# Kernel optimization log

Measured on AMD Instinct MI355X. Metric: run time of the kernel, lower is better.

Reference implementation:

```python
import jax, jax.numpy as jnp
import numpy as np

H = 64  # GRU hidden size


def _gru_scan(x_proj, m, U, b_rec):
    # x_proj: [S,B,3H] precomputed input projections (time-major); m: [S,B] bool mask
    B = x_proj.shape[1]
    h0 = jnp.zeros((B, H), x_proj.dtype)

    def step(h, inp):
        xp, mt = inp
        rec = h @ U + b_rec                       # [B,3H] (Keras reset_after=True)
        xz, xr, xh = jnp.split(xp, 3, axis=-1)
        rz, rr, rh = jnp.split(rec, 3, axis=-1)
        z = jax.nn.sigmoid(xz + rz)
        r = jax.nn.sigmoid(xr + rr)
        hh = jnp.tanh(xh + r * rh)
        hn = z * h + (1.0 - z) * hh
        hn = jnp.where(mt[:, None], hn, h)        # masked steps carry state through
        return hn, hn

    hT, hs = jax.lax.scan(step, h0, (x_proj, m))
    return hs, hT  # hs: [S,B,H], hT: [B,H]


def setup_inputs() -> dict:
    key = jax.random.key(0)
    ks = jax.random.split(key, 16)
    V, E = 50000, 25
    B, S, T = 512, 200, 10
    s = 0.05
    f32 = jnp.float32
    inp = {
        "input_batch": jax.random.randint(ks[0], (B, S, T), 0, V),
        "emb_table": jax.random.normal(ks[1], (V, E), f32) * s,
        "W_f": jax.random.normal(ks[2], (E, 3 * H), f32) * s,
        "U_f": jax.random.normal(ks[3], (H, 3 * H), f32) * s,
        "b_f": jnp.zeros((2, 3 * H), f32),
        "W_b": jax.random.normal(ks[4], (E, 3 * H), f32) * s,
        "U_b": jax.random.normal(ks[5], (H, 3 * H), f32) * s,
        "b_b": jnp.zeros((2, 3 * H), f32),
        "W_k": jax.random.normal(ks[6], (2 * H, H), f32) * s,
        "b_k": jnp.zeros((H,), f32),
        "W_q": jax.random.normal(ks[7], (H, H), f32) * s,
        "b_q": jnp.zeros((H,), f32),
        "W_e": jax.random.normal(ks[8], (H, 1), f32) * s,
        "b_e": jnp.zeros((1,), f32),
    }
    return inp


def reference(input_batch, emb_table, W_f, U_f, b_f, W_b, U_b, b_b, W_k, b_k, W_q, b_q, W_e, b_e):
    mask = input_batch != 0                                  # [B,S,T]
    emb = emb_table[input_batch]                             # [B,S,T,E]
    nm = mask.astype(emb.dtype)
    denom = nm.sum(axis=2)                                   # [B,S]
    denom = jnp.where(denom == 0, jnp.ones_like(denom), denom)
    x = (emb * nm[..., None]).sum(axis=2) / denom[..., None] # [B,S,E] masked mean over tags
    step_mask = mask[:, :, 0]                                # [B,S] GRU step mask

    xT = jnp.swapaxes(x, 0, 1)                               # [S,B,E]
    mT = jnp.swapaxes(step_mask, 0, 1)                       # [S,B]

    # forward GRU
    hs_f, hT_f = _gru_scan(xT @ W_f + b_f[0], mT, U_f, b_f[1])
    # backward GRU: reverse time, scan, reverse back
    hs_b, _ = _gru_scan((xT @ W_b + b_b[0])[::-1], mT[::-1], U_b, b_b[1])
    hs_b = hs_b[::-1]

    out = jnp.swapaxes(jnp.concatenate([hs_f, hs_b], axis=-1), 0, 1)  # [B,S,2H]

    # Bahdanau attention; query = forward final state
    keys = out @ W_k + b_k                                   # [B,S,H]
    queries = hT_f @ W_q + b_q                               # [B,H]
    e = jnp.tanh(keys + queries[:, None, :]) @ W_e + b_e     # [B,S,1]
    e = e + (1.0 - step_mask.astype(e.dtype))[..., None] * -1e9
    w = jax.nn.softmax(e, axis=1)                            # [B,S,1]
    context = (w * out).sum(axis=1)                          # [B,2H]
    return context
```

## Files before the change

### kernel.cpp

```cpp
#include <hip/hip_runtime.h>
#include <math.h>

#define BATCH 512
#define SEQ   200
#define TOK   10
#define EMB   25
#define XPAD  28
#define HID   64
#define G3    192

__device__ __forceinline__ float fast_sigmoid(float t) {
    float e = __expf(-t);
    return __builtin_amdgcn_rcpf(1.f + e);
}
__device__ __forceinline__ float fast_tanh(float t) {
    float e2 = __expf(2.f * t);
    return 1.f - 2.f * __builtin_amdgcn_rcpf(e2 + 1.f);
}

#define LDS_BARRIER() do {                                   \
    asm volatile("s_waitcnt lgkmcnt(0)" ::: "memory");       \
    __builtin_amdgcn_s_barrier();                            \
    asm volatile("" ::: "memory");                           \
} while (0)

__global__ __launch_bounds__(256) void emb_mean_kernel(
    const int* __restrict__ ids_g, const float* __restrict__ emb,
    float* __restrict__ x, float* __restrict__ mask)
{
    int grp  = blockIdx.x * 8 + (threadIdx.x >> 5);
    int lane = threadIdx.x & 31;
    if (grp >= BATCH * SEQ) return;
    const int* ids = ids_g + (size_t)grp * TOK;
    float acc = 0.f;
    int cnt = 0;
    #pragma unroll
    for (int t = 0; t < TOK; t++) {
        int id = ids[t];
        if (id != 0) {
            cnt++;
            if (lane < EMB) acc += emb[(size_t)id * EMB + lane];
        }
    }
    if (lane < EMB)
        x[(size_t)grp * EMB + lane] = cnt ? acc / (float)cnt : 0.f;
    if (lane == 0)
        mask[grp] = (ids[0] != 0) ? 1.f : 0.f;
}


#define U_LIST(M) \
  M(0)  M(1)  M(2)  M(3)  M(4)  M(5)  M(6)  M(7)  \
  M(8)  M(9)  M(10) M(11) M(12) M(13) M(14) M(15) \
  M(16) M(17) M(18) M(19) M(20) M(21) M(22) M(23) \
  M(24) M(25) M(26) M(27) M(28) M(29) M(30) M(31) \
  M(32) M(33) M(34) M(35) M(36) M(37) M(38) M(39) \
  M(40) M(41) M(42) M(43) M(44) M(45) M(46) M(47) \
  M(48) M(49) M(50) M(51) M(52) M(53) M(54) M(55) \
  M(56) M(57) M(58) M(59) M(60) M(61) M(62) M(63)

#define W_LIST(M) \
  M(0)  M(1)  M(2)  M(3)  M(4)  M(5)  M(6)  M(7)  \
  M(8)  M(9)  M(10) M(11) M(12) M(13) M(14) M(15) \
  M(16) M(17) M(18) M(19) M(20) M(21) M(22) M(23) M(24)

#define DECL_U(i) const float u##i = U[(i) * G3 + col];
#define DECL_W(i) const float w##i = W[(i) * G3 + col];

#define REC4(q, i0, i1, i2, i3) {                 \
    const float4 hv = hs4[q];                     \
    a0 = fmaf(hv.x, u##i0, a0);                   \
    a1 = fmaf(hv.y, u##i1, a1);                   \
    a2 = fmaf(hv.z, u##i2, a2);                   \
    a3 = fmaf(hv.w, u##i3, a3); }

#define X4(q, i0, i1, i2, i3) {                   \
    const float4 xv = xr4[q];                     \
    p0 = fmaf(xv.x, w##i0, p0);                   \
    p1 = fmaf(xv.y, w##i1, p1);                   \
    p2 = fmaf(xv.z, w##i2, p2);                   \
    p3 = fmaf(xv.w, w##i3, p3); }

#define XPROJ(P, XR) do {                                         \
    const float4* xr4 = (const float4*)(XR);                      \
    float p0 = bx, p1 = 0.f, p2 = 0.f, p3 = 0.f;                  \
    X4(0, 0, 1, 2, 3)   X4(1, 4, 5, 6, 7)   X4(2, 8, 9, 10, 11)  \
    X4(3, 12, 13, 14, 15) X4(4, 16, 17, 18, 19) X4(5, 20, 21, 22, 23) \
    p0 = fmaf((XR)[24], w24, p0);                                 \
    P = (p0 + p1) + (p2 + p3);                                    \
} while (0)

__global__ __launch_bounds__(192, 3) void gru_kernel(
    const float* __restrict__ xg, const float* __restrict__ maskg,
    const float* __restrict__ W_f, const float* __restrict__ U_f, const float* __restrict__ b_f,
    const float* __restrict__ W_b, const float* __restrict__ U_b, const float* __restrict__ b_b,
    float* __restrict__ outg, float* __restrict__ hT)
{
    const int bidx = blockIdx.x;
    const int dir  = bidx >> 9;
    const int b    = bidx & 511;
    const int tid  = threadIdx.x;
    const int w    = tid >> 6;
    const int j    = tid & 63;

    const float* W    = dir ? W_b : W_f;
    const float* U    = dir ? U_b : U_f;
    const float* bias = dir ? b_b : b_f;

    const int col = w * HID + j;

    U_LIST(DECL_U)
    W_LIST(DECL_W)
    const float bx = bias[col];
    const float br = bias[G3 + col];

    __shared__ __align__(16) float xs[SEQ * XPAD];
    __shared__ float ms[SEQ];
    __shared__ __align__(16) float hs[HID];
    __shared__ float zs[HID];
    __shared__ float rs[HID];

    {
        for (int i = tid; i < SEQ * EMB; i += 192) {
            int s = i / EMB;
            int e = i - s * EMB;
            xs[s * XPAD + e] = xg[(size_t)b * (SEQ * EMB) + i];
        }
        for (int i = tid; i < SEQ; i += 192) ms[i] = maskg[(size_t)b * SEQ + i];
        if (tid < HID) hs[tid] = 0.f;
    }
    __syncthreads();

    const float4* hs4 = (const float4*)hs;
    float h = 0.f;
    float* obase = outg + (size_t)b * SEQ * (2 * HID) + dir * HID + j;

    float p;
    {
        const int s0 = dir ? (SEQ - 1) : 0;
        XPROJ(p, xs + s0 * XPAD);
    }

    for (int step = 0; step < SEQ; step++) {
        const int s = dir ? (SEQ - 1 - step) : step;

        float a0 = br, a1 = 0.f, a2 = 0.f, a3 = 0.f;
        REC4(0,  0,  1,  2,  3)   REC4(1,  4,  5,  6,  7)
        REC4(2,  8,  9, 10, 11)   REC4(3, 12, 13, 14, 15)
        REC4(4, 16, 17, 18, 19)   REC4(5, 20, 21, 22, 23)
        REC4(6, 24, 25, 26, 27)   REC4(7, 28, 29, 30, 31)
        REC4(8, 32, 33, 34, 35)   REC4(9, 36, 37, 38, 39)
        REC4(10, 40, 41, 42, 43)  REC4(11, 44, 45, 46, 47)
        REC4(12, 48, 49, 50, 51)  REC4(13, 52, 53, 54, 55)
        REC4(14, 56, 57, 58, 59)  REC4(15, 60, 61, 62, 63)
        const float a = (a0 + a1) + (a2 + a3);

        if (w == 0)      zs[j] = fast_sigmoid(p + a);
        else if (w == 1) rs[j] = fast_sigmoid(p + a);

        LDS_BARRIER();

        if (w == 2) {
            float r  = rs[j];
            float z  = zs[j];
            float hh = fast_tanh(p + r * a);
            float hn = z * h + (1.f - z) * hh;
            hn = (ms[s] != 0.f) ? hn : h;
            h = hn;
            hs[j] = hn;
            obase[(size_t)s * (2 * HID)] = hn;
        }

        {
            const int sn  = dir ? (SEQ - 2 - step) : (step + 1);
            const int snc = (step + 1 < SEQ) ? sn : s;
            XPROJ(p, xs + snc * XPAD);
        }

        LDS_BARRIER();
    }
    if (w == 2 && dir == 0) hT[(size_t)b * HID + j] = h;
}

__global__ __launch_bounds__(256) void attn_kernel(
    const float* __restrict__ outg, const float* __restrict__ maskg,
    const float* __restrict__ hT,
    const float* __restrict__ W_k, const float* __restrict__ b_k,
    const float* __restrict__ W_q, const float* __restrict__ b_q,
    const float* __restrict__ W_e, const float* __restrict__ b_e,
    float* __restrict__ ctx)
{
    const int b   = blockIdx.x;
    const int tid = threadIdx.x;

    __shared__ float Wks[2 * HID * HID];
    __shared__ float qs[HID];
    __shared__ float es[SEQ];

    for (int i = tid; i < 2 * HID * HID; i += 256) Wks[i] = W_k[i];
    if (tid < HID) {
        float q = b_q[tid];
        const float* hrow = hT + (size_t)b * HID;
        #pragma unroll 8
        for (int i = 0; i < HID; i++) q = fmaf(hrow[i], W_q[i * HID + tid], q);
        qs[tid] = q;
    }
    __syncthreads();

    const int wave = tid >> 6;
    const int lane = tid & 63;
    const float bk = b_k[lane];
    const float we = W_e[lane];
    const float be = b_e[0];

    for (int s = wave; s < SEQ; s += 4) {
        const float* orow = outg + ((size_t)b * SEQ + s) * (2 * HID);
        float a0 = 0.f, a1 = 0.f, a2 = 0.f, a3 = 0.f;
        #pragma unroll
        for (int i = 0; i < 2 * HID; i += 4) {
            a0 = fmaf(orow[i + 0], Wks[(i + 0) * HID + lane], a0);
            a1 = fmaf(orow[i + 1], Wks[(i + 1) * HID + lane], a1);
            a2 = fmaf(orow[i + 2], Wks[(i + 2) * HID + lane], a2);
            a3 = fmaf(orow[i + 3], Wks[(i + 3) * HID + lane], a3);
        }
        float t = tanhf(((a0 + a1) + (a2 + a3)) + bk + qs[lane]) * we;
        #pragma unroll
        for (int off = 32; off > 0; off >>= 1) t += __shfl_down(t, off);
        if (lane == 0) {
            float pen = (maskg[(size_t)b * SEQ + s] != 0.f) ? 0.f : -1e9f;
            es[s] = t + be + pen;
        }
    }
    __syncthreads();

    if (tid < 64) {
        float mx = -1e30f;
        for (int s2 = tid; s2 < SEQ; s2 += 64) mx = fmaxf(mx, es[s2]);
        #pragma unroll
        for (int off = 32; off > 0; off >>= 1) mx = fmaxf(mx, __shfl_xor(mx, off));
        float sum = 0.f;
        for (int s2 = tid; s2 < SEQ; s2 += 64) {
            float w = expf(es[s2] - mx);
            es[s2] = w;
            sum += w;
        }
        #pragma unroll
        for (int off = 32; off > 0; off >>= 1) sum += __shfl_xor(sum, off);
        float inv = 1.f / sum;
        for (int s2 = tid; s2 < SEQ; s2 += 64) es[s2] *= inv;
    }
    __syncthreads();

    if (tid < 2 * HID) {
        const int jj = tid;
        float a0 = 0.f, a1 = 0.f;
        for (int s2 = 0; s2 < SEQ; s2 += 2) {
            a0 = fmaf(es[s2],     outg[((size_t)b * SEQ + s2)     * (2 * HID) + jj], a0);
            a1 = fmaf(es[s2 + 1], outg[((size_t)b * SEQ + s2 + 1) * (2 * HID) + jj], a1);
        }
        ctx[(size_t)b * (2 * HID) + jj] = a0 + a1;
    }
}

extern "C" void kernel_launch(void* const* d_in, const int* in_sizes, int n_in,
                              void* d_out, int out_size, void* d_ws, size_t ws_size,
                              hipStream_t stream) {
    const int*   ids = (const int*)  d_in[0];
    const float* emb = (const float*)d_in[1];
    const float* W_f = (const float*)d_in[2];
    const float* U_f = (const float*)d_in[3];
    const float* b_f = (const float*)d_in[4];
    const float* W_b = (const float*)d_in[5];
    const float* U_b = (const float*)d_in[6];
    const float* b_b = (const float*)d_in[7];
    const float* W_k = (const float*)d_in[8];
    const float* b_k = (const float*)d_in[9];
    const float* W_q = (const float*)d_in[10];
    const float* b_q = (const float*)d_in[11];
    const float* W_e = (const float*)d_in[12];
    const float* b_e = (const float*)d_in[13];

    float* ws   = (float*)d_ws;
    float* x    = ws;
    float* mask = ws + 2560000;
    float* out  = ws + 2662400;
    float* hT   = ws + 15769600;

    emb_mean_kernel<<<(BATCH * SEQ) / 8, 256, 0, stream>>>(ids, emb, x, mask);
    gru_kernel<<<1024, 192, 0, stream>>>(x, mask, W_f, U_f, b_f,
                                         W_b, U_b, b_b, out, hT);
    attn_kernel<<<BATCH, 256, 0, stream>>>(out, mask, hT, W_k, b_k,
                                           W_q, b_q, W_e, b_e, (float*)d_out);
}
```

Before: 431.2 us.

## Keep W_k slices in registers and split attention K-dimension across waves

The attention kernel no longer stages the whole 128x64 W_k matrix in LDS. Each wave holds a 32-row slice of W_k in registers, reads out rows as float4, and writes partial key sums to LDS in tiles of 8 timesteps; the partials are then combined before tanh and the score reduction. The context reduction now uses all four waves with float2 loads and a final LDS sum, where before only 128 threads did it. This removes the LDS fill and the LDS weight reads at the cost of two extra barriers per tile and higher register pressure.

```diff
diff --git a/kernel.cpp b/kernel.cpp
--- a/kernel.cpp
+++ b/kernel.cpp
@@ -8,6 +8,7 @@
 #define XPAD  28
 #define HID   64
 #define G3    192
+#define ATILE 8
 
 __device__ __forceinline__ float fast_sigmoid(float t) {
     float e = __expf(-t);
@@ -182,6 +183,22 @@
     if (w == 2 && dir == 0) hT[(size_t)b * HID + j] = h;
 }
 
+
+#define WK_LIST(M) \
+  M(0)  M(1)  M(2)  M(3)  M(4)  M(5)  M(6)  M(7)  \
+  M(8)  M(9)  M(10) M(11) M(12) M(13) M(14) M(15) \
+  M(16) M(17) M(18) M(19) M(20) M(21) M(22) M(23) \
+  M(24) M(25) M(26) M(27) M(28) M(29) M(30) M(31)
+
+#define DECL_WK(t) const float wk##t = W_k[(size_t)(32 * wave + (t)) * HID + lane];
+
+#define KF4(q, t0, t1, t2, t3) {                  \
+    const float4 ov = o4[q];                      \
+    acc0 = fmaf(ov.x, wk##t0, acc0);              \
+    acc1 = fmaf(ov.y, wk##t1, acc1);              \
+    acc0 = fmaf(ov.z, wk##t2, acc0);              \
+    acc1 = fmaf(ov.w, wk##t3, acc1); }
+
 __global__ __launch_bounds__(256) void attn_kernel(
     const float* __restrict__ outg, const float* __restrict__ maskg,
     const float* __restrict__ hT,
@@ -190,14 +207,22 @@
     const float* __restrict__ W_e, const float* __restrict__ b_e,
     float* __restrict__ ctx)
 {
-    const int b   = blockIdx.x;
-    const int tid = threadIdx.x;
-
-    __shared__ float Wks[2 * HID * HID];
+    const int b    = blockIdx.x;
+    const int tid  = threadIdx.x;
+    const int wave = tid >> 6;
+    const int lane = tid & 63;
+
     __shared__ float qs[HID];
     __shared__ float es[SEQ];
-
-    for (int i = tid; i < 2 * HID * HID; i += 256) Wks[i] = W_k[i];
+    __shared__ __align__(16) float kp[ATILE][4][HID];
+    __shared__ __align__(16) float psum[4][2 * HID];
+
+    WK_LIST(DECL_WK)
+
+    const float bkj = b_k[lane];
+    const float wej = W_e[lane];
+    const float be  = b_e[0];
+
     if (tid < HID) {
         float q = b_q[tid];
         const float* hrow = hT + (size_t)b * HID;
@@ -206,32 +231,37 @@
         qs[tid] = q;
     }
     __syncthreads();
-
-    const int wave = tid >> 6;
-    const int lane = tid & 63;
-    const float bk = b_k[lane];
-    const float we = W_e[lane];
-    const float be = b_e[0];
-
-    for (int s = wave; s < SEQ; s += 4) {
-        const float* orow = outg + ((size_t)b * SEQ + s) * (2 * HID);
-        float a0 = 0.f, a1 = 0.f, a2 = 0.f, a3 = 0.f;
+    const float qj = qs[lane];
+
+    for (int s0 = 0; s0 < SEQ; s0 += ATILE) {
+        #pragma unroll 2
+        for (int t = 0; t < ATILE; t++) {
+            const int s = s0 + t;
+            const float4* o4 = (const float4*)(outg +
+                ((size_t)b * SEQ + s) * (2 * HID) + 32 * wave);
+            float acc0 = 0.f, acc1 = 0.f;
+            KF4(0,  0,  1,  2,  3)  KF4(1,  4,  5,  6,  7)
+            KF4(2,  8,  9, 10, 11)  KF4(3, 12, 13, 14, 15)
+            KF4(4, 16, 17, 18, 19)  KF4(5, 20, 21, 22, 23)
+            KF4(6, 24, 25, 26, 27)  KF4(7, 28, 29, 30, 31)
+            kp[t][wave][lane] = acc0 + acc1;
+        }
+        __syncthreads();
         #pragma unroll
-        for (int i = 0; i < 2 * HID; i += 4) {
-            a0 = fmaf(orow[i + 0], Wks[(i + 0) * HID + lane], a0);
-            a1 = fmaf(orow[i + 1], Wks[(i + 1) * HID + lane], a1);
-            a2 = fmaf(orow[i + 2], Wks[(i + 2) * HID + lane], a2);
-            a3 = fmaf(orow[i + 3], Wks[(i + 3) * HID + lane], a3);
-        }
-        float t = tanhf(((a0 + a1) + (a2 + a3)) + bk + qs[lane]) * we;
-        #pragma unroll
-        for (int off = 32; off > 0; off >>= 1) t += __shfl_down(t, off);
-        if (lane == 0) {
-            float pen = (maskg[(size_t)b * SEQ + s] != 0.f) ? 0.f : -1e9f;
-            es[s] = t + be + pen;
-        }
-    }
-    __syncthreads();
+        for (int t = wave; t < ATILE; t += 4) {
+            const int s = s0 + t;
+            float k = (kp[t][0][lane] + kp[t][1][lane]) +
+                      (kp[t][2][lane] + kp[t][3][lane]);
+            float v = tanhf(k + bkj + qj) * wej;
+            #pragma unroll
+            for (int off = 32; off > 0; off >>= 1) v += __shfl_xor(v, off);
+            if (lane == 0) {
+                float pen = (maskg[(size_t)b * SEQ + s] != 0.f) ? 0.f : -1e9f;
+                es[s] = v + be + pen;
+            }
+        }
+        __syncthreads();
+    }
 
     if (tid < 64) {
         float mx = -1e30f;
@@ -251,14 +281,23 @@
     }
     __syncthreads();
 
+    {
+        float a0 = 0.f, a1 = 0.f;
+        #pragma unroll 2
+        for (int s2 = wave; s2 < SEQ; s2 += 4) {
+            const float2 v = *(const float2*)(outg +
+                ((size_t)b * SEQ + s2) * (2 * HID) + lane * 2);
+            const float wsc = es[s2];
+            a0 = fmaf(wsc, v.x, a0);
+            a1 = fmaf(wsc, v.y, a1);
+        }
+        psum[wave][2 * lane]     = a0;
+        psum[wave][2 * lane + 1] = a1;
+    }
+    __syncthreads();
     if (tid < 2 * HID) {
-        const int jj = tid;
-        float a0 = 0.f, a1 = 0.f;
-        for (int s2 = 0; s2 < SEQ; s2 += 2) {
-            a0 = fmaf(es[s2],     outg[((size_t)b * SEQ + s2)     * (2 * HID) + jj], a0);
-            a1 = fmaf(es[s2 + 1], outg[((size_t)b * SEQ + s2 + 1) * (2 * HID) + jj], a1);
-        }
-        ctx[(size_t)b * (2 * HID) + jj] = a0 + a1;
+        ctx[(size_t)b * (2 * HID) + tid] =
+            (psum[0][tid] + psum[1][tid]) + (psum[2][tid] + psum[3][tid]);
     }
 }
 
```

New measurement: 430.4 us (median of 2 runs). Within noise of the previous version (-0.2%).
